# Optimization experiments

Measured on AMD Instinct MI355X. Metric: run time of the kernel, lower is better.

The kernel has to match this reference:

```python
import jax, jax.numpy as jnp
import numpy as np

B, S, H = 8, 4096, 2048
DH = 64            # selector hidden dim
K = 256            # num_perturb_tokens (min(K, S) = 256)
SCALE = 0.1        # perturbation_scale
FIXED_TYPE = 1     # type_values[1] == 0.0
TYPE_VALUES = jnp.array([-1.0, 0.0, 1.0], dtype=jnp.float32)


def setup_inputs() -> dict:
    key = jax.random.key(0)
    k_hs, k_u, k_w1, k_w2 = jax.random.split(key, 4)
    hidden_states = jax.random.normal(k_hs, (B, S, H), dtype=jnp.float32)
    # torch.rand_like -> uniform [0,1); keep strictly >0 so -log(-log(u)) is finite
    noise_u = jax.random.uniform(k_u, (B, S), dtype=jnp.float32, minval=1e-9, maxval=1.0)
    w1 = jax.random.normal(k_w1, (H, DH), dtype=jnp.float32) * 0.02
    b1 = jnp.zeros((DH,), dtype=jnp.float32)
    w2 = jax.random.normal(k_w2, (DH, 1), dtype=jnp.float32) * 0.02
    b2 = jnp.zeros((1,), dtype=jnp.float32)
    return {"hidden_states": hidden_states, "noise_u": noise_u,
            "w1": w1, "b1": b1, "w2": w2, "b2": b2}


def reference(hidden_states, noise_u, w1, b1, w2, b2):
    hs = hidden_states.astype(jnp.float32)                       # (B,S,H)
    # TokenSelectorNetwork: Linear -> ReLU -> Linear -> squeeze(-1)
    h = jax.nn.relu(jnp.einsum('bsh,hd->bsd', hs, w1) + b1)       # (B,S,DH)
    selection_logits = (jnp.einsum('bsd,do->bso', h, w2) + b2)[..., 0]  # (B,S)

    # gumbel-perturbed top-k token selection (deterministic=False path)
    gumbel = -jnp.log(-jnp.log(noise_u))
    _, selected_indices = jax.lax.top_k(selection_logits + gumbel, K)   # (B,K)

    # log prob of selection (gather from log-softmax, mean over K)
    log_probs_all = jax.nn.log_softmax(selection_logits, axis=-1)       # (B,S)
    log_prob = jnp.take_along_axis(log_probs_all, selected_indices, axis=1).mean(axis=-1)  # (B,)

    # fixed perturbation type -> constant perturb values, scattered over selected rows
    perturb_types = jnp.full((B, K), FIXED_TYPE, dtype=jnp.int32)
    perturb_values = TYPE_VALUES[perturb_types] * SCALE                 # (B,K), all zeros here
    expanded_values = jnp.broadcast_to(perturb_values[..., None], (B, K, H))
    sel_clamped = jnp.clip(selected_indices, 0, S - 1)
    batch_idx = jnp.arange(B)[:, None]                                  # (B,1)
    perturbed = hs.at[batch_idx, sel_clamped].set(expanded_values)      # scatter_ along dim 1

    return (perturbed.astype(jnp.float16), selected_indices, perturb_types, log_prob)
```

## Files before the change

kernel.cpp:

```cpp
#include <hip/hip_runtime.h>
#include <hip/hip_fp16.h>

#define NB 8
#define NS 4096
#define NH 2048
#define NDH 64
#define NK 256
#define BK 32
#define MT 128
#define KS 4
#define KCH (NH / KS)

__global__ __launch_bounds__(128, 2) void k_sel_gemm(
    const float* __restrict__ hs, const float* __restrict__ w1,
    float* __restrict__ out0, float* __restrict__ part)
{
    __shared__ float As[MT][BK + 4];
    __shared__ float Ws[BK][NDH];

    const int tid = threadIdx.x;
    const int tx = tid & 7;
    const int ty = tid >> 3;
    const int tile = blockIdx.x & 255;
    const int kc = blockIdx.x >> 8;
    const int tokenBase = tile * MT;
    const int kBase = kc * KCH;

    float acc[8][8];
#pragma unroll
    for (int t = 0; t < 8; ++t)
#pragma unroll
        for (int j = 0; j < 8; ++j) acc[t][j] = 0.0f;

    for (int ko = 0; ko < KCH; ko += BK) {
#pragma unroll
        for (int r = 0; r < 8; ++r) {
            const int f = r * 128 + tid;
            const int tok = f >> 3;
            const int k4 = (f & 7) * 4;
            const long long gi = (long long)(tokenBase + tok) * NH + kBase + ko + k4;
            const float4 v = *reinterpret_cast<const float4*>(hs + gi);
            float4 o;
            o.x = __half2float(__float2half(v.x));
            o.y = __half2float(__float2half(v.y));
            o.z = __half2float(__float2half(v.z));
            o.w = __half2float(__float2half(v.w));
            *reinterpret_cast<float4*>(out0 + gi) = o;
            *reinterpret_cast<float4*>(&As[tok][k4]) = v;
        }
#pragma unroll
        for (int r = 0; r < 4; ++r) {
            const int f = r * 128 + tid;
            const int row = f >> 4;
            const int col = (f & 15) * 4;
            *reinterpret_cast<float4*>(&Ws[row][col]) =
                *reinterpret_cast<const float4*>(w1 + (long long)(kBase + ko + row) * NDH + col);
        }
        __syncthreads();

#pragma unroll
        for (int kk = 0; kk < BK; kk += 4) {
            float4 av[8];
#pragma unroll
            for (int t = 0; t < 8; ++t)
                av[t] = *reinterpret_cast<const float4*>(&As[ty + 16 * t][kk]);
#pragma unroll
            for (int i = 0; i < 4; ++i) {
                const float4 w0 = *reinterpret_cast<const float4*>(&Ws[kk + i][tx * 8]);
                const float4 w1v = *reinterpret_cast<const float4*>(&Ws[kk + i][tx * 8 + 4]);
#pragma unroll
                for (int t = 0; t < 8; ++t) {
                    const float a = reinterpret_cast<const float*>(&av[t])[i];
                    acc[t][0] += a * w0.x;  acc[t][1] += a * w0.y;
                    acc[t][2] += a * w0.z;  acc[t][3] += a * w0.w;
                    acc[t][4] += a * w1v.x; acc[t][5] += a * w1v.y;
                    acc[t][6] += a * w1v.z; acc[t][7] += a * w1v.w;
                }
            }
        }
        __syncthreads();
    }

#pragma unroll
    for (int t = 0; t < 8; ++t) {
        const long long o =
            ((long long)kc * (NB * NS) + tokenBase + ty + 16 * t) * NDH + tx * 8;
        const float4 lo = make_float4(acc[t][0], acc[t][1], acc[t][2], acc[t][3]);
        const float4 hi = make_float4(acc[t][4], acc[t][5], acc[t][6], acc[t][7]);
        *reinterpret_cast<float4*>(part + o) = lo;
        *reinterpret_cast<float4*>(part + o + 4) = hi;
    }
}

__global__ __launch_bounds__(256) void k_reduce(
    const float* __restrict__ part, const float* __restrict__ b1,
    const float* __restrict__ w2, const float* __restrict__ b2,
    float* __restrict__ logits)
{
    const int T = blockIdx.x * 4 + (threadIdx.x >> 6);
    const int lane = threadIdx.x & 63;
    float s = 0.0f;
#pragma unroll
    for (int kc = 0; kc < KS; ++kc)
        s += part[((long long)kc * (NB * NS) + T) * NDH + lane];
    const float h = fmaxf(s + b1[lane], 0.0f);
    float p = h * w2[lane];
#pragma unroll
    for (int m = 1; m < 64; m <<= 1) p += __shfl_xor(p, m, 64);
    if (lane == 0) logits[T] = p + b2[0];
}

__global__ __launch_bounds__(1024) void k_topk(
    const float* __restrict__ logits, const float* __restrict__ noise,
    float* __restrict__ outIdx, float* __restrict__ outType,
    float* __restrict__ outLP, int* __restrict__ wsIdx)
{
    __shared__ unsigned int ukey[NS];
    __shared__ float rawl[NS];
    __shared__ unsigned int hist[256];
    __shared__ unsigned int sufx[256];
    __shared__ float red[1024];
    __shared__ unsigned int candU[512];
    __shared__ int candIdx[512];
    __shared__ int sel[NK];
    __shared__ unsigned int misc[3];

    const int b = blockIdx.x;
    const int tid = threadIdx.x;

    for (int e = tid; e < NS; e += 1024) {
        const float l = logits[b * NS + e];
        const float u = noise[b * NS + e];
        const float g = -logf(-logf(u));
        unsigned int x = __float_as_uint(l + g);
        x = (x & 0x80000000u) ? ~x : (x | 0x80000000u);
        ukey[e] = x;
        rawl[e] = l;
    }
    if (tid == 0) { misc[0] = 0u; misc[1] = NK; misc[2] = 0u; }
    __syncthreads();

    for (int pass = 0; pass < 4; ++pass) {
        const int shift = 24 - pass * 8;
        if (tid < 256) hist[tid] = 0u;
        __syncthreads();
        const unsigned int pfx = misc[0];
        for (int e = tid; e < NS; e += 1024) {
            const unsigned int x = ukey[e];
            if (pass == 0 || (x >> (shift + 8)) == pfx)
                atomicAdd(&hist[(x >> shift) & 255u], 1u);
        }
        __syncthreads();
        if (tid < 256) sufx[tid] = hist[tid];
        __syncthreads();
        for (int off = 1; off < 256; off <<= 1) {
            unsigned int v = 0u;
            if (tid < 256) v = sufx[tid] + ((tid + off < 256) ? sufx[tid + off] : 0u);
            __syncthreads();
            if (tid < 256) sufx[tid] = v;
            __syncthreads();
        }
        const unsigned int rem = misc[1];
        if (tid < 256) {
            const unsigned int ge = sufx[tid];
            const unsigned int gt = (tid < 255) ? sufx[tid + 1] : 0u;
            if (ge >= rem && gt < rem) {
                misc[0] = (pfx << 8) | (unsigned int)tid;
                misc[1] = rem - gt;
            }
        }
        __syncthreads();
    }

    const unsigned int T = misc[0];
    for (int e = tid; e < NS; e += 1024) {
        if (ukey[e] >= T) {
            const unsigned int slot = atomicAdd(&misc[2], 1u);
            if (slot < 512u) { candU[slot] = ukey[e]; candIdx[slot] = e; }
        }
    }
    __syncthreads();
    const int C = (int)min(misc[2], 512u);

    for (int c = tid; c < C; c += 1024) {
        const unsigned int xu = candU[c];
        const int xi = candIdx[c];
        int r = 0;
        for (int j = 0; j < C; ++j) {
            const unsigned int yu = candU[j];
            r += (int)((yu > xu) || (yu == xu && candIdx[j] < xi));
        }
        if (r < NK) {
            outIdx[b * NK + r] = (float)xi;
            outType[b * NK + r] = 1.0f;
            wsIdx[b * NK + r] = xi;
            sel[r] = xi;
        }
    }

    float lm = -INFINITY;
    for (int e = tid; e < NS; e += 1024) lm = fmaxf(lm, rawl[e]);
    red[tid] = lm;
    __syncthreads();
    for (int s2 = 512; s2 > 0; s2 >>= 1) {
        if (tid < s2) red[tid] = fmaxf(red[tid], red[tid + s2]);
        __syncthreads();
    }
    const float maxv = red[0];
    __syncthreads();
    float ls = 0.0f;
    for (int e = tid; e < NS; e += 1024) ls += expf(rawl[e] - maxv);
    red[tid] = ls;
    __syncthreads();
    for (int s2 = 512; s2 > 0; s2 >>= 1) {
        if (tid < s2) red[tid] += red[tid + s2];
        __syncthreads();
    }
    const float lse = logf(red[0]);
    __syncthreads();

    float contrib = (tid < NK) ? (rawl[sel[tid]] - maxv - lse) : 0.0f;
    red[tid] = contrib;
    __syncthreads();
    for (int s2 = 512; s2 > 0; s2 >>= 1) {
        if (tid < s2) red[tid] += red[tid + s2];
        __syncthreads();
    }
    if (tid == 0) outLP[b] = red[0] / (float)NK;
}

__global__ __launch_bounds__(256) void k_zero_rows(
    const int* __restrict__ wsIdx, float* __restrict__ out0)
{
    const int blk = blockIdx.x;
    const int b = blk >> 8;
    const int r = blk & 255;
    const int row = wsIdx[b * NK + r];
    const float4 z = make_float4(0.f, 0.f, 0.f, 0.f);
    float4* p = reinterpret_cast<float4*>(out0 + ((long long)(b * NS + row)) * NH);
    p[threadIdx.x]       = z;
    p[threadIdx.x + 256] = z;
}

extern "C" void kernel_launch(void* const* d_in, const int* in_sizes, int n_in,
                              void* d_out, int out_size, void* d_ws, size_t ws_size,
                              hipStream_t stream) {
    const float* hs    = (const float*)d_in[0];
    const float* noise = (const float*)d_in[1];
    const float* w1    = (const float*)d_in[2];
    const float* b1    = (const float*)d_in[3];
    const float* w2    = (const float*)d_in[4];
    const float* b2    = (const float*)d_in[5];

    float* out0    = (float*)d_out;
    float* outIdx  = out0 + (long long)NB * NS * NH;
    float* outType = outIdx + NB * NK;
    float* outLP   = outType + NB * NK;

    float* logits = (float*)d_ws;
    int*   wsIdx  = (int*)d_ws + NB * NS;
    float* part   = (float*)d_ws + NB * NS + NB * NK;

    k_sel_gemm<<<256 * KS, 128, 0, stream>>>(hs, w1, out0, part);
    k_reduce<<<NB * NS / 4, 256, 0, stream>>>(part, b1, w2, b2, logits);
    k_topk<<<NB, 1024, 0, stream>>>(logits, noise, outIdx, outType, outLP, wsIdx);
    k_zero_rows<<<NB * NK, 256, 0, stream>>>(wsIdx, out0);
}
```

Baseline: 516.4 us.

## Register-prefetch GEMM tiles with 256 threads; shrink top-k block and use wave shuffles

The selector GEMM now runs 256 threads per block, each holding a 4x8 accumulator tile. The next k-slice of hidden states and weights is prefetched into registers while the current slice is computed, so global load latency overlaps the FMA work. The fp16 copy of the output is written from those prefetched registers. The top-k kernel drops from 1024 to 256 threads, and its suffix scans and reductions use wavefront shuffles instead of shared-memory trees with many barriers. The trade-off is more register pressure in the GEMM and fewer threads in the histogram loops of top-k.

```diff
diff --git a/kernel.cpp b/kernel.cpp
--- a/kernel.cpp
+++ b/kernel.cpp
@@ -11,7 +11,7 @@
 #define KS 4
 #define KCH (NH / KS)
 
-__global__ __launch_bounds__(128, 2) void k_sel_gemm(
+__global__ __launch_bounds__(256, 4) void k_sel_gemm(
     const float* __restrict__ hs, const float* __restrict__ w1,
     float* __restrict__ out0, float* __restrict__ part)
 {
@@ -26,50 +26,67 @@
     const int tokenBase = tile * MT;
     const int kBase = kc * KCH;
 
-    float acc[8][8];
-#pragma unroll
-    for (int t = 0; t < 8; ++t)
+    const int sK = (tid & 7) * 4;
+    const long long aBase = (long long)(tokenBase + ty) * NH + kBase + sK;
+    const int wRow = tid >> 4;
+    const int wCol = (tid & 15) * 4;
+    const float* wBase = w1 + (long long)(kBase + wRow) * NDH + wCol;
+
+    float acc[4][8];
+#pragma unroll
+    for (int t = 0; t < 4; ++t)
 #pragma unroll
         for (int j = 0; j < 8; ++j) acc[t][j] = 0.0f;
 
+    float4 va[4], wv[2];
+#pragma unroll
+    for (int r = 0; r < 4; ++r)
+        va[r] = *reinterpret_cast<const float4*>(hs + aBase + (long long)r * 32 * NH);
+#pragma unroll
+    for (int r = 0; r < 2; ++r)
+        wv[r] = *reinterpret_cast<const float4*>(wBase + (long long)(r * 16) * NDH);
+
     for (int ko = 0; ko < KCH; ko += BK) {
 #pragma unroll
-        for (int r = 0; r < 8; ++r) {
-            const int f = r * 128 + tid;
-            const int tok = f >> 3;
-            const int k4 = (f & 7) * 4;
-            const long long gi = (long long)(tokenBase + tok) * NH + kBase + ko + k4;
-            const float4 v = *reinterpret_cast<const float4*>(hs + gi);
+        for (int r = 0; r < 4; ++r)
+            *reinterpret_cast<float4*>(&As[ty + r * 32][sK]) = va[r];
+#pragma unroll
+        for (int r = 0; r < 2; ++r)
+            *reinterpret_cast<float4*>(&Ws[wRow + r * 16][wCol]) = wv[r];
+        __syncthreads();
+
+#pragma unroll
+        for (int r = 0; r < 4; ++r) {
             float4 o;
-            o.x = __half2float(__float2half(v.x));
-            o.y = __half2float(__float2half(v.y));
-            o.z = __half2float(__float2half(v.z));
-            o.w = __half2float(__float2half(v.w));
-            *reinterpret_cast<float4*>(out0 + gi) = o;
-            *reinterpret_cast<float4*>(&As[tok][k4]) = v;
-        }
-#pragma unroll
-        for (int r = 0; r < 4; ++r) {
-            const int f = r * 128 + tid;
-            const int row = f >> 4;
-            const int col = (f & 15) * 4;
-            *reinterpret_cast<float4*>(&Ws[row][col]) =
-                *reinterpret_cast<const float4*>(w1 + (long long)(kBase + ko + row) * NDH + col);
-        }
-        __syncthreads();
+            o.x = __half2float(__float2half(va[r].x));
+            o.y = __half2float(__float2half(va[r].y));
+            o.z = __half2float(__float2half(va[r].z));
+            o.w = __half2float(__float2half(va[r].w));
+            *reinterpret_cast<float4*>(out0 + aBase + ko + (long long)r * 32 * NH) = o;
+        }
+        if (ko + BK < KCH) {
+#pragma unroll
+            for (int r = 0; r < 4; ++r)
+                va[r] = *reinterpret_cast<const float4*>(
+                    hs + aBase + (ko + BK) + (long long)r * 32 * NH);
+#pragma unroll
+            for (int r = 0; r < 2; ++r)
+                wv[r] = *reinterpret_cast<const float4*>(
+                    wBase + (long long)(ko + BK + r * 16) * NDH);
+        }
 
 #pragma unroll
         for (int kk = 0; kk < BK; kk += 4) {
-            float4 av[8];
-#pragma unroll
-            for (int t = 0; t < 8; ++t)
-                av[t] = *reinterpret_cast<const float4*>(&As[ty + 16 * t][kk]);
+            float4 av[4];
+#pragma unroll
+            for (int t = 0; t < 4; ++t)
+                av[t] = *reinterpret_cast<const float4*>(&As[ty + 32 * t][kk]);
 #pragma unroll
             for (int i = 0; i < 4; ++i) {
                 const float4 w0 = *reinterpret_cast<const float4*>(&Ws[kk + i][tx * 8]);
                 const float4 w1v = *reinterpret_cast<const float4*>(&Ws[kk + i][tx * 8 + 4]);
 #pragma unroll
-                for (int t = 0; t < 8; ++t) {
+                for (int t = 0; t < 4; ++t) {
                     const float a = reinterpret_cast<const float*>(&av[t])[i];
                     acc[t][0] += a * w0.x;  acc[t][1] += a * w0.y;
                     acc[t][2] += a * w0.z;  acc[t][3] += a * w0.w;
@@ -82,13 +99,13 @@
     }
 
 #pragma unroll
-    for (int t = 0; t < 8; ++t) {
+    for (int t = 0; t < 4; ++t) {
         const long long o =
-            ((long long)kc * (NB * NS) + tokenBase + ty + 16 * t) * NDH + tx * 8;
-        const float4 lo = make_float4(acc[t][0], acc[t][1], acc[t][2], acc[t][3]);
-        const float4 hi = make_float4(acc[t][4], acc[t][5], acc[t][6], acc[t][7]);
-        *reinterpret_cast<float4*>(part + o) = lo;
-        *reinterpret_cast<float4*>(part + o + 4) = hi;
+            ((long long)kc * (NB * NS) + tokenBase + ty + 32 * t) * NDH + tx * 8;
+        *reinterpret_cast<float4*>(part + o) =
+            make_float4(acc[t][0], acc[t][1], acc[t][2], acc[t][3]);
+        *reinterpret_cast<float4*>(part + o + 4) =
+            make_float4(acc[t][4], acc[t][5], acc[t][6], acc[t][7]);
     }
 }
 
@@ -110,7 +127,7 @@
     if (lane == 0) logits[T] = p + b2[0];
 }
 
-__global__ __launch_bounds__(1024) void k_topk(
+__global__ __launch_bounds__(256) void k_topk(
     const float* __restrict__ logits, const float* __restrict__ noise,
     float* __restrict__ outIdx, float* __restrict__ outType,
     float* __restrict__ outLP, int* __restrict__ wsIdx)
@@ -118,17 +135,18 @@
     __shared__ unsigned int ukey[NS];
     __shared__ float rawl[NS];
     __shared__ unsigned int hist[256];
-    __shared__ unsigned int sufx[256];
-    __shared__ float red[1024];
     __shared__ unsigned int candU[512];
     __shared__ int candIdx[512];
     __shared__ int sel[NK];
+    __shared__ float redw[4];
     __shared__ unsigned int misc[3];
 
     const int b = blockIdx.x;
     const int tid = threadIdx.x;
-
-    for (int e = tid; e < NS; e += 1024) {
+    const int lane = tid & 63;
+    const int wid = tid >> 6;
+
+    for (int e = tid; e < NS; e += 256) {
         const float l = logits[b * NS + e];
         const float u = noise[b * NS + e];
         const float g = -logf(-logf(u));
@@ -142,38 +160,48 @@
 
     for (int pass = 0; pass < 4; ++pass) {
         const int shift = 24 - pass * 8;
-        if (tid < 256) hist[tid] = 0u;
+        hist[tid] = 0u;
         __syncthreads();
         const unsigned int pfx = misc[0];
-        for (int e = tid; e < NS; e += 1024) {
+        const unsigned int rem = misc[1];
+        for (int e = tid; e < NS; e += 256) {
             const unsigned int x = ukey[e];
             if (pass == 0 || (x >> (shift + 8)) == pfx)
                 atomicAdd(&hist[(x >> shift) & 255u], 1u);
         }
         __syncthreads();
-        if (tid < 256) sufx[tid] = hist[tid];
-        __syncthreads();
-        for (int off = 1; off < 256; off <<= 1) {
-            unsigned int v = 0u;
-            if (tid < 256) v = sufx[tid] + ((tid + off < 256) ? sufx[tid + off] : 0u);
-            __syncthreads();
-            if (tid < 256) sufx[tid] = v;
-            __syncthreads();
-        }
-        const unsigned int rem = misc[1];
-        if (tid < 256) {
-            const unsigned int ge = sufx[tid];
-            const unsigned int gt = (tid < 255) ? sufx[tid + 1] : 0u;
-            if (ge >= rem && gt < rem) {
-                misc[0] = (pfx << 8) | (unsigned int)tid;
-                misc[1] = rem - gt;
+        if (tid < 64) {
+            const unsigned int h0 = hist[4 * tid];
+            const unsigned int h1 = hist[4 * tid + 1];
+            const unsigned int h2 = hist[4 * tid + 2];
+            const unsigned int h3 = hist[4 * tid + 3];
+            const unsigned int g = h0 + h1 + h2 + h3;
+            unsigned int s = g;
+#pragma unroll
+            for (int m = 1; m < 64; m <<= 1) {
+                const unsigned int v = __shfl_down(s, m, 64);
+                if (tid + m < 64) s += v;
             }
+            const unsigned int Snext = s - g;
+            const unsigned int s3 = Snext + h3;
+            const unsigned int s2 = s3 + h2;
+            const unsigned int s1 = s2 + h1;
+            const unsigned int s0 = s1 + h0;
+            const unsigned int ge[4] = { s0, s1, s2, s3 };
+            const unsigned int gt[4] = { s1, s2, s3, Snext };
+#pragma unroll
+            for (int i = 0; i < 4; ++i) {
+                if (ge[i] >= rem && gt[i] < rem) {
+                    misc[0] = (pfx << 8) | (unsigned int)(4 * tid + i);
+                    misc[1] = rem - gt[i];
+                }
+            }
         }
         __syncthreads();
     }
 
     const unsigned int T = misc[0];
-    for (int e = tid; e < NS; e += 1024) {
+    for (int e = tid; e < NS; e += 256) {
         if (ukey[e] >= T) {
             const unsigned int slot = atomicAdd(&misc[2], 1u);
             if (slot < 512u) { candU[slot] = ukey[e]; candIdx[slot] = e; }
@@ -182,7 +210,7 @@
     __syncthreads();
     const int C = (int)min(misc[2], 512u);
 
-    for (int c = tid; c < C; c += 1024) {
+    for (int c = tid; c < C; c += 256) {
         const unsigned int xu = candU[c];
         const int xi = candIdx[c];
         int r = 0;
@@ -199,34 +227,27 @@
     }
 
     float lm = -INFINITY;
-    for (int e = tid; e < NS; e += 1024) lm = fmaxf(lm, rawl[e]);
-    red[tid] = lm;
-    __syncthreads();
-    for (int s2 = 512; s2 > 0; s2 >>= 1) {
-        if (tid < s2) red[tid] = fmaxf(red[tid], red[tid + s2]);
-        __syncthreads();
-    }
-    const float maxv = red[0];
+    for (int e = tid; e < NS; e += 256) lm = fmaxf(lm, rawl[e]);
+#pragma unroll
+    for (int m = 32; m; m >>= 1) lm = fmaxf(lm, __shfl_xor(lm, m, 64));
+    if (lane == 0) redw[wid] = lm;
+    __syncthreads();
+    const float maxv = fmaxf(fmaxf(redw[0], redw[1]), fmaxf(redw[2], redw[3]));
     __syncthreads();
     float ls = 0.0f;
-    for (int e = tid; e < NS; e += 1024) ls += expf(rawl[e] - maxv);
-    red[tid] = ls;
-    __syncthreads();
-    for (int s2 = 512; s2 > 0; s2 >>= 1) {
-        if (tid < s2) red[tid] += red[tid + s2];
-        __syncthreads();
-    }
-    const float lse = logf(red[0]);
-    __syncthreads();
-
-    float contrib = (tid < NK) ? (rawl[sel[tid]] - maxv - lse) : 0.0f;
-    red[tid] = contrib;
-    __syncthreads();
-    for (int s2 = 512; s2 > 0; s2 >>= 1) {
-        if (tid < s2) red[tid] += red[tid + s2];
-        __syncthreads();
-    }
-    if (tid == 0) outLP[b] = red[0] / (float)NK;
+    for (int e = tid; e < NS; e += 256) ls += expf(rawl[e] - maxv);
+#pragma unroll
+    for (int m = 32; m; m >>= 1) ls += __shfl_xor(ls, m, 64);
+    if (lane == 0) redw[wid] = ls;
+    __syncthreads();
+    const float lse = logf(redw[0] + redw[1] + redw[2] + redw[3]);
+    __syncthreads();
+    float contrib = rawl[sel[tid]] - maxv - lse;
+#pragma unroll
+    for (int m = 32; m; m >>= 1) contrib += __shfl_xor(contrib, m, 64);
+    if (lane == 0) redw[wid] = contrib;
+    __syncthreads();
+    if (tid == 0) outLP[b] = (redw[0] + redw[1] + redw[2] + redw[3]) / (float)NK;
 }
 
 __global__ __launch_bounds__(256) void k_zero_rows(
@@ -261,8 +282,8 @@
     int*   wsIdx  = (int*)d_ws + NB * NS;
     float* part   = (float*)d_ws + NB * NS + NB * NK;
 
-    k_sel_gemm<<<256 * KS, 128, 0, stream>>>(hs, w1, out0, part);
+    k_sel_gemm<<<256 * KS, 256, 0, stream>>>(hs, w1, out0, part);
     k_reduce<<<NB * NS / 4, 256, 0, stream>>>(part, b1, w2, b2, logits);
-    k_topk<<<NB, 1024, 0, stream>>>(logits, noise, outIdx, outType, outLP, wsIdx);
+    k_topk<<<NB, 256, 0, stream>>>(logits, noise, outIdx, outType, outLP, wsIdx);
     k_zero_rows<<<NB * NK, 256, 0, stream>>>(wsIdx, out0);
 }
```

Result: slower. 721.9 us (+39.8%).
